# Optimization experiments

Measured on AMD Instinct MI355X. Metric: run time of the kernel, lower is better.

The kernel has to match this reference:

```python
import jax, jax.numpy as jnp
import numpy as np

N_NODES = 100000
N_EDGES = 1600000
N_FEAT = 64
DIM = 32
N_CLASSES = 10
N_GRAPHS = 64
BN_EPS = 1e-5


def setup_inputs() -> dict:
    key = jax.random.key(0)
    ks = jax.random.split(key, 20)
    x = jax.random.normal(ks[0], (N_NODES, N_FEAT), dtype=jnp.float32)
    edge_index = jax.random.randint(ks[1], (2, N_EDGES), 0, N_NODES, dtype=jnp.int64)
    batch = jnp.sort(jax.random.randint(ks[2], (N_NODES,), 0, N_GRAPHS, dtype=jnp.int64))
    s = 0.1
    # conv1 MLP (in=N_FEAT)
    w1a = jax.random.normal(ks[3], (N_FEAT, DIM), dtype=jnp.float32) * s
    b1a = jnp.zeros((DIM,), jnp.float32)
    w1b = jax.random.normal(ks[4], (DIM, DIM), dtype=jnp.float32) * s
    b1b = jnp.zeros((DIM,), jnp.float32)
    # convs 2-5 MLPs stacked [4, DIM, DIM]
    Wa = jax.random.normal(ks[5], (4, DIM, DIM), dtype=jnp.float32) * s
    Ba = jnp.zeros((4, DIM), jnp.float32)
    Wb = jax.random.normal(ks[6], (4, DIM, DIM), dtype=jnp.float32) * s
    Bb = jnp.zeros((4, DIM), jnp.float32)
    bn_gamma = jnp.ones((5, DIM), jnp.float32)
    bn_beta = jnp.zeros((5, DIM), jnp.float32)
    fc1_w = jax.random.normal(ks[7], (DIM, DIM), dtype=jnp.float32) * s
    fc1_b = jnp.zeros((DIM,), jnp.float32)
    fc2_w = jax.random.normal(ks[8], (DIM, N_CLASSES), dtype=jnp.float32) * s
    fc2_b = jnp.zeros((N_CLASSES,), jnp.float32)
    return dict(x=x, edge_index=edge_index, batch=batch,
                w1a=w1a, b1a=b1a, w1b=w1b, b1b=b1b,
                Wa=Wa, Ba=Ba, Wb=Wb, Bb=Bb,
                bn_gamma=bn_gamma, bn_beta=bn_beta,
                fc1_w=fc1_w, fc1_b=fc1_b, fc2_w=fc2_w, fc2_b=fc2_b)


def _gin_aggr(x, src, dst):
    # sum_{j in N(i)} x_j  + x_i   (eps = 0)
    agg = jax.ops.segment_sum(x[src], dst, num_segments=N_NODES)
    return x + agg


def _mlp(h, wa, ba, wb, bb):
    return jax.nn.relu(h @ wa + ba) @ wb + bb


def _bn(h, gamma, beta):
    mu = jnp.mean(h, axis=0)
    var = jnp.mean((h - mu) ** 2, axis=0)  # biased, torch BN training mode
    return (h - mu) * jax.lax.rsqrt(var + BN_EPS) * gamma + beta


def reference(x, edge_index, batch, w1a, b1a, w1b, b1b, Wa, Ba, Wb, Bb,
              bn_gamma, bn_beta, fc1_w, fc1_b, fc2_w, fc2_b):
    src, dst = edge_index[0], edge_index[1]
    # layer 1 (num_features -> dim)
    h = _mlp(_gin_aggr(x, src, dst), w1a, b1a, w1b, b1b)
    h = _bn(jax.nn.relu(h), bn_gamma[0], bn_beta[0])
    # layers 2-5 (dim -> dim)
    for i in range(4):
        h = _mlp(_gin_aggr(h, src, dst), Wa[i], Ba[i], Wb[i], Bb[i])
        h = _bn(jax.nn.relu(h), bn_gamma[i + 1], bn_beta[i + 1])
    # global add pool over graphs
    g = jax.ops.segment_sum(h, batch, num_segments=N_GRAPHS)  # [G, dim]
    g = jax.nn.relu(g @ fc1_w + fc1_b)
    # dropout: eval mode -> identity
    return g @ fc2_w + fc2_b  # [G, num_classes]
```

## Files before the change

kernel.cpp:

```cpp
#include <hip/hip_runtime.h>
#include <hip/hip_fp16.h>

#define NN 100000
#define NE 1600000
#define NF 64
#define DM 32
#define NG 64
#define NC 10
#define BN_EPS 1e-5f

#define BSHIFT 8
#define NBUCK ((NN + 255) >> 8)
#define CHUNK 8192
#define NCH ((NE + CHUNK - 1) / CHUNK)

__device__ __forceinline__ float2 up2(unsigned u) {
    __half2 h = __builtin_bit_cast(__half2, u);
    return __half22float2(h);
}
__device__ __forceinline__ unsigned pk2(float a, float b) {
    __half2 h = __floats2half2_rn(a, b);
    return __builtin_bit_cast(unsigned, h);
}

__global__ __launch_bounds__(256) void binA_k(const int* __restrict__ ei,
                                              int* __restrict__ bcnt) {
    __shared__ int h[NBUCK];
    for (int i = threadIdx.x; i < NBUCK; i += 256) h[i] = 0;
    __syncthreads();
    long long base = (long long)blockIdx.x * CHUNK;
    int n = (int)((NE - base < CHUNK) ? (NE - base) : CHUNK);
    for (int i = threadIdx.x; i < n; i += 256) {
        int d = ei[NE + base + i];
        atomicAdd(&h[d >> BSHIFT], 1);
    }
    __syncthreads();
    for (int i = threadIdx.x; i < NBUCK; i += 256)
        if (h[i]) atomicAdd(&bcnt[i], h[i]);
}

__global__ __launch_bounds__(512) void binB_k(const int* __restrict__ bcnt,
                                              int* __restrict__ bbase,
                                              int* __restrict__ bcur) {
    __shared__ int s[512];
    int t = threadIdx.x;
    int v = (t < NBUCK) ? bcnt[t] : 0;
    s[t] = v;
    __syncthreads();
    int acc = v;
    for (int off = 1; off < 512; off <<= 1) {
        int add = (t >= off) ? s[t - off] : 0;
        __syncthreads();
        acc += add;
        s[t] = acc;
        __syncthreads();
    }
    if (t < NBUCK) { bbase[t] = acc - v; bcur[t] = acc - v; }
    if (t == 0) bbase[NBUCK] = NE;
}

__global__ __launch_bounds__(256) void binC_k(const int* __restrict__ ei,
                                              int* __restrict__ bcur,
                                              unsigned* __restrict__ binned) {
    __shared__ int cnt[NBUCK];
    __shared__ int ofs[NBUCK];
    __shared__ int idx[NBUCK];
    for (int i = threadIdx.x; i < NBUCK; i += 256) { cnt[i] = 0; idx[i] = 0; }
    __syncthreads();
    long long base = (long long)blockIdx.x * CHUNK;
    int n = (int)((NE - base < CHUNK) ? (NE - base) : CHUNK);
    int d[CHUNK / 256];
#pragma unroll
    for (int k = 0; k < CHUNK / 256; k++) {
        int i = threadIdx.x + k * 256;
        int dd = (i < n) ? ei[NE + base + i] : -1;
        d[k] = dd;
        if (dd >= 0) atomicAdd(&cnt[dd >> BSHIFT], 1);
    }
    __syncthreads();
    for (int i = threadIdx.x; i < NBUCK; i += 256)
        if (cnt[i]) ofs[i] = atomicAdd(&bcur[i], cnt[i]);
    __syncthreads();
#pragma unroll
    for (int k = 0; k < CHUNK / 256; k++) {
        int i = threadIdx.x + k * 256;
        if (i < n) {
            unsigned src = (unsigned)ei[base + i];
            int b = d[k] >> BSHIFT;
            int l = atomicAdd(&idx[b], 1);
            binned[ofs[b] + l] = (src << 8) | (unsigned)(d[k] & 255);
        }
    }
}

__global__ __launch_bounds__(256) void binD_k(const unsigned* __restrict__ binned,
                                              const int* __restrict__ bbase,
                                              int* __restrict__ rowptr,
                                              int* __restrict__ csr) {
    __shared__ int cnt[256];
    __shared__ int cur[256];
    __shared__ int s[256];
    int b = blockIdx.x;
    int e0 = bbase[b], e1 = bbase[b + 1];
    int t = threadIdx.x;
    cnt[t] = 0;
    __syncthreads();
    for (int e = e0 + t; e < e1; e += 256) atomicAdd(&cnt[binned[e] & 255u], 1);
    __syncthreads();
    int v = cnt[t];
    s[t] = v;
    __syncthreads();
    int acc = v;
    for (int off = 1; off < 256; off <<= 1) {
        int add = (t >= off) ? s[t - off] : 0;
        __syncthreads();
        acc += add;
        s[t] = acc;
        __syncthreads();
    }
    int base = e0 + acc - v;
    int node = (b << BSHIFT) + t;
    if (node < NN) rowptr[node] = base;
    cur[t] = base;
    if (b == NBUCK - 1 && t == 0) rowptr[NN] = NE;
    __syncthreads();
    for (int e = e0 + t; e < e1; e += 256) {
        unsigned w = binned[e];
        int p = atomicAdd(&cur[w & 255u], 1);
        csr[p] = (int)(w >> 8);
    }
}

__global__ __launch_bounds__(256) void pre1_k(const float* __restrict__ x,
                                              const float* __restrict__ wa,
                                              float* __restrict__ y,
                                              unsigned* __restrict__ yhf,
                                              float* __restrict__ zbuf) {
    __shared__ float sWa[64 * 32];
    int tid = threadIdx.x;
    if (blockIdx.x == 0) {
        for (int i = tid; i < 5 * 64 + NG * 32; i += 256) zbuf[i] = 0.f;
    }
    for (int i = tid; i < 64 * 32; i += 256) sWa[i] = wa[i];
    __syncthreads();
    int l = tid & 3;
    int node = blockIdx.x * 64 + (tid >> 2);
    if (node >= NN) return;
    float t[8];
#pragma unroll
    for (int j = 0; j < 8; j++) t[j] = 0.f;
    const float4* xr = reinterpret_cast<const float4*>(x + (long long)node * 64);
    const float4* w4 = reinterpret_cast<const float4*>(sWa);
#pragma unroll
    for (int k4 = 0; k4 < 16; k4++) {
        float4 xv = xr[k4];
        float av[4] = {xv.x, xv.y, xv.z, xv.w};
#pragma unroll
        for (int i = 0; i < 4; i++) {
            float a = av[i];
            float4 w0 = w4[(k4 * 4 + i) * 8 + 2 * l];
            float4 w1 = w4[(k4 * 4 + i) * 8 + 2 * l + 1];
            t[0] += a * w0.x; t[1] += a * w0.y; t[2] += a * w0.z; t[3] += a * w0.w;
            t[4] += a * w1.x; t[5] += a * w1.y; t[6] += a * w1.z; t[7] += a * w1.w;
        }
    }
    float4* yr = reinterpret_cast<float4*>(y + (long long)node * 32 + l * 8);
    float4 o0, o1;
    o0.x = t[0]; o0.y = t[1]; o0.z = t[2]; o0.w = t[3];
    o1.x = t[4]; o1.y = t[5]; o1.z = t[6]; o1.w = t[7];
    yr[0] = o0; yr[1] = o1;
    uint4 p;
    p.x = pk2(t[0], t[1]); p.y = pk2(t[2], t[3]);
    p.z = pk2(t[4], t[5]); p.w = pk2(t[6], t[7]);
    reinterpret_cast<uint4*>(yhf)[(long long)node * 4 + l] = p;
}

template <bool BN>
__global__ __launch_bounds__(256) void gatherH_k(const unsigned* __restrict__ thf,
                                                 const int* __restrict__ rowptr,
                                                 const int* __restrict__ csr,
                                                 float* __restrict__ agg,
                                                 const float* __restrict__ st,
                                                 const float* __restrict__ gamma,
                                                 const float* __restrict__ beta) {
    int tid = threadIdx.x;
    int node = blockIdx.x * 64 + (tid >> 2);
    int l = tid & 3;
    if (node >= NN) return;
    float sc[8], sh[8];
    if (BN) {
        const float invn = 1.0f / NN;
#pragma unroll
        for (int c = 0; c < 8; c++) {
            int f = 8 * l + c;
            float mu = st[f] * invn;
            float var = st[32 + f] * invn - mu * mu;
            float scale = rsqrtf(var + BN_EPS) * gamma[f];
            sc[c] = scale;
            sh[c] = beta[f] - mu * scale;
        }
    }
    int s = rowptr[node], e = rowptr[node + 1];
    const uint4* t4 = reinterpret_cast<const uint4*>(thf);
    float a[8];
#pragma unroll
    for (int c = 0; c < 8; c++) a[c] = 0.f;
    int i = s;
    for (; i + 4 <= e; i += 4) {
        int s0 = csr[i], s1 = csr[i + 1], s2 = csr[i + 2], s3 = csr[i + 3];
        uint4 w0 = t4[(long long)s0 * 4 + l];
        uint4 w1 = t4[(long long)s1 * 4 + l];
        uint4 w2 = t4[(long long)s2 * 4 + l];
        uint4 w3 = t4[(long long)s3 * 4 + l];
        float2 p;
        p = up2(w0.x); a[0] += p.x; a[1] += p.y;
        p = up2(w0.y); a[2] += p.x; a[3] += p.y;
        p = up2(w0.z); a[4] += p.x; a[5] += p.y;
        p = up2(w0.w); a[6] += p.x; a[7] += p.y;
        p = up2(w1.x); a[0] += p.x; a[1] += p.y;
        p = up2(w1.y); a[2] += p.x; a[3] += p.y;
        p = up2(w1.z); a[4] += p.x; a[5] += p.y;
        p = up2(w1.w); a[6] += p.x; a[7] += p.y;
        p = up2(w2.x); a[0] += p.x; a[1] += p.y;
        p = up2(w2.y); a[2] += p.x; a[3] += p.y;
        p = up2(w2.z); a[4] += p.x; a[5] += p.y;
        p = up2(w2.w); a[6] += p.x; a[7] += p.y;
        p = up2(w3.x); a[0] += p.x; a[1] += p.y;
        p = up2(w3.y); a[2] += p.x; a[3] += p.y;
        p = up2(w3.z); a[4] += p.x; a[5] += p.y;
        p = up2(w3.w); a[6] += p.x; a[7] += p.y;
    }
    for (; i < e; i++) {
        uint4 w = t4[(long long)csr[i] * 4 + l];
        float2 p;
        p = up2(w.x); a[0] += p.x; a[1] += p.y;
        p = up2(w.y); a[2] += p.x; a[3] += p.y;
        p = up2(w.z); a[4] += p.x; a[5] += p.y;
        p = up2(w.w); a[6] += p.x; a[7] += p.y;
    }
    if (BN) {
        float deg = (float)(e - s);
#pragma unroll
        for (int c = 0; c < 8; c++) a[c] = a[c] * sc[c] + deg * sh[c];
    }
    float4* ar = reinterpret_cast<float4*>(agg + (long long)node * 32 + l * 8);
    float4 o0, o1;
    o0.x = a[0]; o0.y = a[1]; o0.z = a[2]; o0.w = a[3];
    o1.x = a[4]; o1.y = a[5]; o1.z = a[6]; o1.w = a[7];
    ar[0] = o0;
    ar[1] = o1;
}

__global__ __launch_bounds__(256) void mlp1b_k(const float* __restrict__ y,
                                               const float* __restrict__ agg,
                                               const float* __restrict__ ba,
                                               const float* __restrict__ wb,
                                               const float* __restrict__ bb,
                                               float* __restrict__ out,
                                               unsigned* __restrict__ outhf,
                                               float* __restrict__ stats) {
    __shared__ float sWb[32 * 32];
    __shared__ float sBa[32], sBb[32];
    __shared__ float sSum[4 * 32], sSq[4 * 32];
    int tid = threadIdx.x;
    for (int i = tid; i < 32 * 32; i += 256) sWb[i] = wb[i];
    if (tid < 32) { sBa[tid] = ba[tid]; sBb[tid] = bb[tid]; }
    __syncthreads();

    int l = tid & 3;
    int node = blockIdx.x * 64 + (tid >> 2);
    bool act = node < NN;
    float t[8];
    if (act) {
        const float4* yr = reinterpret_cast<const float4*>(y + (long long)node * 32 + l * 8);
        const float4* ar = reinterpret_cast<const float4*>(agg + (long long)node * 32 + l * 8);
        float4 y0 = yr[0], y1 = yr[1], a0 = ar[0], a1 = ar[1];
        t[0] = fmaxf(y0.x + a0.x + sBa[l * 8 + 0], 0.f);
        t[1] = fmaxf(y0.y + a0.y + sBa[l * 8 + 1], 0.f);
        t[2] = fmaxf(y0.z + a0.z + sBa[l * 8 + 2], 0.f);
        t[3] = fmaxf(y0.w + a0.w + sBa[l * 8 + 3], 0.f);
        t[4] = fmaxf(y1.x + a1.x + sBa[l * 8 + 4], 0.f);
        t[5] = fmaxf(y1.y + a1.y + sBa[l * 8 + 5], 0.f);
        t[6] = fmaxf(y1.z + a1.z + sBa[l * 8 + 6], 0.f);
        t[7] = fmaxf(y1.w + a1.w + sBa[l * 8 + 7], 0.f);
    } else {
#pragma unroll
        for (int j = 0; j < 8; j++) t[j] = 0.f;
    }

    float r[8];
#pragma unroll
    for (int j = 0; j < 8; j++) r[j] = sBb[l * 8 + j];
    const float4* v4 = reinterpret_cast<const float4*>(sWb);
#pragma unroll
    for (int k = 0; k < 32; k++) {
        float a = __shfl(t[k & 7], k >> 3, 4);
        float4 w0 = v4[k * 8 + 2 * l];
        float4 w1 = v4[k * 8 + 2 * l + 1];
        r[0] += a * w0.x; r[1] += a * w0.y; r[2] += a * w0.z; r[3] += a * w0.w;
        r[4] += a * w1.x; r[5] += a * w1.y; r[6] += a * w1.z; r[7] += a * w1.w;
    }
#pragma unroll
    for (int j = 0; j < 8; j++) r[j] = fmaxf(r[j], 0.f);

    if (act) {
        float4* orow = reinterpret_cast<float4*>(out + (long long)node * 32 + l * 8);
        float4 o0, o1;
        o0.x = r[0]; o0.y = r[1]; o0.z = r[2]; o0.w = r[3];
        o1.x = r[4]; o1.y = r[5]; o1.z = r[6]; o1.w = r[7];
        orow[0] = o0; orow[1] = o1;
        uint4 p;
        p.x = pk2(r[0], r[1]); p.y = pk2(r[2], r[3]);
        p.z = pk2(r[4], r[5]); p.w = pk2(r[6], r[7]);
        reinterpret_cast<uint4*>(outhf)[(long long)node * 4 + l] = p;
    } else {
#pragma unroll
        for (int j = 0; j < 8; j++) r[j] = 0.f;
    }

    int lane = tid & 63, wid = tid >> 6;
#pragma unroll
    for (int j = 0; j < 8; j++) {
        float v = r[j], v2 = v * v;
        v += __shfl_down(v, 32, 64); v2 += __shfl_down(v2, 32, 64);
        v += __shfl_down(v, 16, 64); v2 += __shfl_down(v2, 16, 64);
        v += __shfl_down(v, 8, 64);  v2 += __shfl_down(v2, 8, 64);
        v += __shfl_down(v, 4, 64);  v2 += __shfl_down(v2, 4, 64);
        if (lane < 4) { sSum[wid * 32 + lane * 8 + j] = v; sSq[wid * 32 + lane * 8 + j] = v2; }
    }
    __syncthreads();
    if (tid < 32) {
        float a = sSum[tid] + sSum[32 + tid] + sSum[64 + tid] + sSum[96 + tid];
        float b = sSq[tid] + sSq[32 + tid] + sSq[64 + tid] + sSq[96 + tid];
        atomicAdd(&stats[tid], a);
        atomicAdd(&stats[32 + tid], b);
    }
}

__global__ __launch_bounds__(256) void mlp32_bn_k(float* __restrict__ h,
                                                  unsigned* __restrict__ hhf,
                                                  const float* __restrict__ agg,
                                                  const float* __restrict__ wa,
                                                  const float* __restrict__ ba,
                                                  const float* __restrict__ wb,
                                                  const float* __restrict__ bb,
                                                  const float* __restrict__ st,
                                                  const float* __restrict__ gamma,
                                                  const float* __restrict__ beta,
                                                  float* __restrict__ statsOut) {
    __shared__ float sWa[32 * 32];
    __shared__ float sWb[32 * 32];
    __shared__ float sBa[32], sBb[32];
    __shared__ float sSc[32], sSh[32];
    __shared__ float sSum[4 * 32], sSq[4 * 32];
    int tid = threadIdx.x;
    for (int i = tid; i < 32 * 32; i += 256) { sWa[i] = wa[i]; sWb[i] = wb[i]; }
    if (tid < 32) {
        sBa[tid] = ba[tid]; sBb[tid] = bb[tid];
        const float invn = 1.0f / NN;
        float mu = st[tid] * invn;
        float var = st[32 + tid] * invn - mu * mu;
        float scale = rsqrtf(var + BN_EPS) * gamma[tid];
        sSc[tid] = scale;
        sSh[tid] = beta[tid] - mu * scale;
    }
    __syncthreads();

    int l = tid & 3;
    int node = blockIdx.x * 64 + (tid >> 2);
    bool act = node < NN;
    float t[8];
    const float4* w4a = reinterpret_cast<const float4*>(sWa);
    if (act) {
        float a[32];
        const float4* hr = reinterpret_cast<const float4*>(h + (long long)node * 32);
        const float4* ar = reinterpret_cast<const float4*>(agg + (long long)node * 32);
#pragma unroll
        for (int k4 = 0; k4 < 8; k4++) {
            float4 xv = hr[k4];
            float4 av = ar[k4];
            a[k4 * 4 + 0] = xv.x * sSc[k4 * 4 + 0] + sSh[k4 * 4 + 0] + av.x;
            a[k4 * 4 + 1] = xv.y * sSc[k4 * 4 + 1] + sSh[k4 * 4 + 1] + av.y;
            a[k4 * 4 + 2] = xv.z * sSc[k4 * 4 + 2] + sSh[k4 * 4 + 2] + av.z;
            a[k4 * 4 + 3] = xv.w * sSc[k4 * 4 + 3] + sSh[k4 * 4 + 3] + av.w;
        }
#pragma unroll
        for (int j = 0; j < 8; j++) t[j] = sBa[l * 8 + j];
#pragma unroll
        for (int k = 0; k < 32; k++) {
            float av = a[k];
            float4 w0 = w4a[k * 8 + 2 * l];
            float4 w1 = w4a[k * 8 + 2 * l + 1];
            t[0] += av * w0.x; t[1] += av * w0.y; t[2] += av * w0.z; t[3] += av * w0.w;
            t[4] += av * w1.x; t[5] += av * w1.y; t[6] += av * w1.z; t[7] += av * w1.w;
        }
#pragma unroll
        for (int j = 0; j < 8; j++) t[j] = fmaxf(t[j], 0.f);
    } else {
#pragma unroll
        for (int j = 0; j < 8; j++) t[j] = 0.f;
    }

    float r[8];
#pragma unroll
    for (int j = 0; j < 8; j++) r[j] = sBb[l * 8 + j];
    const float4* v4 = reinterpret_cast<const float4*>(sWb);
#pragma unroll
    for (int k = 0; k < 32; k++) {
        float a = __shfl(t[k & 7], k >> 3, 4);
        float4 w0 = v4[k * 8 + 2 * l];
        float4 w1 = v4[k * 8 + 2 * l + 1];
        r[0] += a * w0.x; r[1] += a * w0.y; r[2] += a * w0.z; r[3] += a * w0.w;
        r[4] += a * w1.x; r[5] += a * w1.y; r[6] += a * w1.z; r[7] += a * w1.w;
    }
#pragma unroll
    for (int j = 0; j < 8; j++) r[j] = fmaxf(r[j], 0.f);

    if (act) {
        float4* orow = reinterpret_cast<float4*>(h + (long long)node * 32 + l * 8);
        float4 o0, o1;
        o0.x = r[0]; o0.y = r[1]; o0.z = r[2]; o0.w = r[3];
        o1.x = r[4]; o1.y = r[5]; o1.z = r[6]; o1.w = r[7];
        orow[0] = o0; orow[1] = o1;
        uint4 p;
        p.x = pk2(r[0], r[1]); p.y = pk2(r[2], r[3]);
        p.z = pk2(r[4], r[5]); p.w = pk2(r[6], r[7]);
        reinterpret_cast<uint4*>(hhf)[(long long)node * 4 + l] = p;
    } else {
#pragma unroll
        for (int j = 0; j < 8; j++) r[j] = 0.f;
    }

    int lane = tid & 63, wid = tid >> 6;
#pragma unroll
    for (int j = 0; j < 8; j++) {
        float v = r[j], v2 = v * v;
        v += __shfl_down(v, 32, 64); v2 += __shfl_down(v2, 32, 64);
        v += __shfl_down(v, 16, 64); v2 += __shfl_down(v2, 16, 64);
        v += __shfl_down(v, 8, 64);  v2 += __shfl_down(v2, 8, 64);
        v += __shfl_down(v, 4, 64);  v2 += __shfl_down(v2, 4, 64);
        if (lane < 4) { sSum[wid * 32 + lane * 8 + j] = v; sSq[wid * 32 + lane * 8 + j] = v2; }
    }
    __syncthreads();
    if (tid < 32) {
        float a = sSum[tid] + sSum[32 + tid] + sSum[64 + tid] + sSum[96 + tid];
        float b = sSq[tid] + sSq[32 + tid] + sSq[64 + tid] + sSq[96 + tid];
        atomicAdd(&statsOut[tid], a);
        atomicAdd(&statsOut[32 + tid], b);
    }
}

#define POOL_NPB 512
__global__ __launch_bounds__(256) void pool_bn_k(const float* __restrict__ h,
                                                 const int* __restrict__ batch,
                                                 const float* __restrict__ st,
                                                 const float* __restrict__ gamma,
                                                 const float* __restrict__ beta,
                                                 float* __restrict__ pooled) {
    int tid = threadIdx.x;
    int f = tid & 31;
    int p = tid >> 5;
    int n0 = blockIdx.x * POOL_NPB + p * (POOL_NPB / 8);
    int n1 = n0 + POOL_NPB / 8;
    if (n1 > NN) n1 = NN;
    if (n0 >= NN) return;
    const float invn = 1.0f / NN;
    float mu = st[f] * invn;
    float var = st[32 + f] * invn - mu * mu;
    float sc = rsqrtf(var + BN_EPS) * gamma[f];
    float sh = beta[f] - mu * sc;
    float acc = 0.f;
    int cur = batch[n0];
    for (int n = n0; n < n1; n++) {
        int g = batch[n];
        if (g != cur) {
            atomicAdd(&pooled[cur * 32 + f], acc);
            cur = g;
            acc = 0.f;
        }
        acc += h[(long long)n * 32 + f] * sc + sh;
    }
    atomicAdd(&pooled[cur * 32 + f], acc);
}

__global__ __launch_bounds__(64) void final_k(const float* __restrict__ pooled,
                                              const float* __restrict__ w1,
                                              const float* __restrict__ b1,
                                              const float* __restrict__ w2,
                                              const float* __restrict__ b2,
                                              float* __restrict__ out) {
    int g = threadIdx.x;
    if (g >= NG) return;
    float t[32];
#pragma unroll
    for (int j = 0; j < 32; j++) t[j] = b1[j];
    for (int k = 0; k < 32; k++) {
        float a = pooled[g * 32 + k];
#pragma unroll
        for (int j = 0; j < 32; j++) t[j] += a * w1[k * 32 + j];
    }
#pragma unroll
    for (int j = 0; j < 32; j++) t[j] = fmaxf(t[j], 0.f);
    for (int c = 0; c < NC; c++) {
        float o = b2[c];
#pragma unroll
        for (int k = 0; k < 32; k++) o += t[k] * w2[k * NC + c];
        out[g * NC + c] = o;
    }
}

extern "C" void kernel_launch(void* const* d_in, const int* in_sizes, int n_in,
                              void* d_out, int out_size, void* d_ws, size_t ws_size,
                              hipStream_t stream) {
    const float* x = (const float*)d_in[0];
    const int* ei = (const int*)d_in[1];
    const int* batch = (const int*)d_in[2];
    const float* w1a = (const float*)d_in[3];
    const float* b1a = (const float*)d_in[4];
    const float* w1b = (const float*)d_in[5];
    const float* b1b = (const float*)d_in[6];
    const float* Wa = (const float*)d_in[7];
    const float* Ba = (const float*)d_in[8];
    const float* Wb = (const float*)d_in[9];
    const float* Bb = (const float*)d_in[10];
    const float* bn_gamma = (const float*)d_in[11];
    const float* bn_beta = (const float*)d_in[12];
    const float* fc1w = (const float*)d_in[13];
    const float* fc1b = (const float*)d_in[14];
    const float* fc2w = (const float*)d_in[15];
    const float* fc2b = (const float*)d_in[16];
    float* out = (float*)d_out;

    float* ws = (float*)d_ws;
    float* y = ws;
    float* hb = y + (size_t)NN * 32;
    float* agg = hb + (size_t)NN * 32;
    float* stats_all = agg + (size_t)NN * 32;
    float* pooled = stats_all + 5 * 64;
    unsigned* yhf = (unsigned*)(pooled + NG * 32);
    unsigned* hbhf = yhf + (size_t)NN * 16;
    unsigned* binned = hbhf + (size_t)NN * 16;
    int* bcnt = (int*)(binned + NE);
    int* bbase = bcnt + NBUCK;
    int* bcur = bbase + NBUCK + 1;
    int* rowptr = bcur + NBUCK;
    int* csr = rowptr + NN + 1;

    const int nb4 = (NN + 63) / 64;

    hipMemsetAsync(bcnt, 0, NBUCK * sizeof(int), stream);
    binA_k<<<NCH, 256, 0, stream>>>(ei, bcnt);
    binB_k<<<1, 512, 0, stream>>>(bcnt, bbase, bcur);
    binC_k<<<NCH, 256, 0, stream>>>(ei, bcur, binned);
    binD_k<<<NBUCK, 256, 0, stream>>>(binned, bbase, rowptr, csr);

    pre1_k<<<nb4, 256, 0, stream>>>(x, w1a, y, yhf, stats_all);
    gatherH_k<false><<<nb4, 256, 0, stream>>>(yhf, rowptr, csr, agg,
                                              nullptr, nullptr, nullptr);
    mlp1b_k<<<nb4, 256, 0, stream>>>(y, agg, b1a, w1b, b1b, hb, hbhf, stats_all);

    for (int i = 0; i < 4; i++) {
        const float* st = stats_all + i * 64;
        const float* g = bn_gamma + i * 32;
        const float* be = bn_beta + i * 32;
        gatherH_k<true><<<nb4, 256, 0, stream>>>(hbhf, rowptr, csr, agg, st, g, be);
        mlp32_bn_k<<<nb4, 256, 0, stream>>>(hb, hbhf, agg, Wa + i * 1024, Ba + i * 32,
                                            Wb + i * 1024, Bb + i * 32,
                                            st, g, be, stats_all + (i + 1) * 64);
    }

    pool_bn_k<<<(NN + POOL_NPB - 1) / POOL_NPB, 256, 0, stream>>>(
        hb, batch, stats_all + 4 * 64, bn_gamma + 4 * 32, bn_beta + 4 * 32, pooled);
    final_k<<<1, 64, 0, stream>>>(pooled, fc1w, fc1b, fc2w, fc2b, out);
}
```

Measured before the change: 584.0 us.

## Fuse neighbor gather with per-layer MLP and BN into one kernel

Merges the CSR gather kernel with the following MLP/BN kernel for every layer, so the aggregated features stay in registers and shared memory instead of being written to and re-read from a global agg buffer. The fp16 gather tables are ping-ponged between two buffers because each layer now reads one table while writing the next. The node's 32-wide input row is staged through a padded shared-memory transpose for the matvecs. This saves one fp32 round trip of the activations and one launch per layer. In exchange each block holds more shared memory and registers, and adds extra barriers between the gather and the MLP phases.

```diff
diff --git a/kernel.cpp b/kernel.cpp
--- a/kernel.cpp
+++ b/kernel.cpp
@@ -175,36 +175,57 @@
     reinterpret_cast<uint4*>(yhf)[(long long)node * 4 + l] = p;
 }
 
-template <bool BN>
-__global__ __launch_bounds__(256) void gatherH_k(const unsigned* __restrict__ thf,
-                                                 const int* __restrict__ rowptr,
-                                                 const int* __restrict__ csr,
-                                                 float* __restrict__ agg,
-                                                 const float* __restrict__ st,
-                                                 const float* __restrict__ gamma,
-                                                 const float* __restrict__ beta) {
+#define SSTR 65
+template <int MODE>
+__global__ __launch_bounds__(256) void fused_k(const float* __restrict__ selfRow,
+                                               float* __restrict__ hOut,
+                                               const unsigned* __restrict__ tblIn,
+                                               unsigned* __restrict__ tblOut,
+                                               const int* __restrict__ rowptr,
+                                               const int* __restrict__ csr,
+                                               const float* __restrict__ wa,
+                                               const float* __restrict__ ba,
+                                               const float* __restrict__ wb,
+                                               const float* __restrict__ bb,
+                                               const float* __restrict__ stPrev,
+                                               const float* __restrict__ gammaPrev,
+                                               const float* __restrict__ betaPrev,
+                                               float* __restrict__ statsOut) {
+    __shared__ float sWa[32 * 32];
+    __shared__ float sWb[32 * 32];
+    __shared__ float sBa[32], sBb[32];
+    __shared__ float sSc[32], sSh[32];
+    __shared__ float sStage[32 * SSTR];
+    __shared__ float sSum[4 * 32], sSq[4 * 32];
     int tid = threadIdx.x;
-    int node = blockIdx.x * 64 + (tid >> 2);
+    for (int i = tid; i < 32 * 32; i += 256) {
+        sWb[i] = wb[i];
+        if (MODE) sWa[i] = wa[i];
+    }
+    if (tid < 32) {
+        sBa[tid] = ba[tid];
+        sBb[tid] = bb[tid];
+        if (MODE) {
+            const float invn = 1.0f / NN;
+            float mu = stPrev[tid] * invn;
+            float var = stPrev[32 + tid] * invn - mu * mu;
+            float scale = rsqrtf(var + BN_EPS) * gammaPrev[tid];
+            sSc[tid] = scale;
+            sSh[tid] = betaPrev[tid] - mu * scale;
+        }
+    }
+
     int l = tid & 3;
-    if (node >= NN) return;
-    float sc[8], sh[8];
-    if (BN) {
-        const float invn = 1.0f / NN;
-#pragma unroll
-        for (int c = 0; c < 8; c++) {
-            int f = 8 * l + c;
-            float mu = st[f] * invn;
-            float var = st[32 + f] * invn - mu * mu;
-            float scale = rsqrtf(var + BN_EPS) * gamma[f];
-            sc[c] = scale;
-            sh[c] = beta[f] - mu * scale;
-        }
-    }
-    int s = rowptr[node], e = rowptr[node + 1];
-    const uint4* t4 = reinterpret_cast<const uint4*>(thf);
-    float a[8];
-#pragma unroll
-    for (int c = 0; c < 8; c++) a[c] = 0.f;
+    int nl = tid >> 2;
+    int node = blockIdx.x * 64 + nl;
+    bool act = node < NN;
+
+    int s = 0, e = 0;
+    if (act) { s = rowptr[node]; e = rowptr[node + 1]; }
+    const uint4* t4 = reinterpret_cast<const uint4*>(tblIn);
+    float g[8];
+#pragma unroll
+    for (int c = 0; c < 8; c++) g[c] = 0.f;
     int i = s;
     for (; i + 4 <= e; i += 4) {
         int s0 = csr[i], s1 = csr[i + 1], s2 = csr[i + 2], s3 = csr[i + 3];
@@ -213,90 +234,92 @@
         uint4 w2 = t4[(long long)s2 * 4 + l];
         uint4 w3 = t4[(long long)s3 * 4 + l];
         float2 p;
-        p = up2(w0.x); a[0] += p.x; a[1] += p.y;
-        p = up2(w0.y); a[2] += p.x; a[3] += p.y;
-        p = up2(w0.z); a[4] += p.x; a[5] += p.y;
-        p = up2(w0.w); a[6] += p.x; a[7] += p.y;
-        p = up2(w1.x); a[0] += p.x; a[1] += p.y;
-        p = up2(w1.y); a[2] += p.x; a[3] += p.y;
-        p = up2(w1.z); a[4] += p.x; a[5] += p.y;
-        p = up2(w1.w); a[6] += p.x; a[7] += p.y;
-        p = up2(w2.x); a[0] += p.x; a[1] += p.y;
-        p = up2(w2.y); a[2] += p.x; a[3] += p.y;
-        p = up2(w2.z); a[4] += p.x; a[5] += p.y;
-        p = up2(w2.w); a[6] += p.x; a[7] += p.y;
-        p = up2(w3.x); a[0] += p.x; a[1] += p.y;
-        p = up2(w3.y); a[2] += p.x; a[3] += p.y;
-        p = up2(w3.z); a[4] += p.x; a[5] += p.y;
-        p = up2(w3.w); a[6] += p.x; a[7] += p.y;
+        p = up2(w0.x); g[0] += p.x; g[1] += p.y;
+        p = up2(w0.y); g[2] += p.x; g[3] += p.y;
+        p = up2(w0.z); g[4] += p.x; g[5] += p.y;
+        p = up2(w0.w); g[6] += p.x; g[7] += p.y;
+        p = up2(w1.x); g[0] += p.x; g[1] += p.y;
+        p = up2(w1.y); g[2] += p.x; g[3] += p.y;
+        p = up2(w1.z); g[4] += p.x; g[5] += p.y;
+        p = up2(w1.w); g[6] += p.x; g[7] += p.y;
+        p = up2(w2.x); g[0] += p.x; g[1] += p.y;
+        p = up2(w2.y); g[2] += p.x; g[3] += p.y;
+        p = up2(w2.z); g[4] += p.x; g[5] += p.y;
+        p = up2(w2.w); g[6] += p.x; g[7] += p.y;
+        p = up2(w3.x); g[0] += p.x; g[1] += p.y;
+        p = up2(w3.y); g[2] += p.x; g[3] += p.y;
+        p = up2(w3.z); g[4] += p.x; g[5] += p.y;
+        p = up2(w3.w); g[6] += p.x; g[7] += p.y;
     }
     for (; i < e; i++) {
         uint4 w = t4[(long long)csr[i] * 4 + l];
         float2 p;
-        p = up2(w.x); a[0] += p.x; a[1] += p.y;
-        p = up2(w.y); a[2] += p.x; a[3] += p.y;
-        p = up2(w.z); a[4] += p.x; a[5] += p.y;
-        p = up2(w.w); a[6] += p.x; a[7] += p.y;
-    }
-    if (BN) {
-        float deg = (float)(e - s);
-#pragma unroll
-        for (int c = 0; c < 8; c++) a[c] = a[c] * sc[c] + deg * sh[c];
-    }
-    float4* ar = reinterpret_cast<float4*>(agg + (long long)node * 32 + l * 8);
-    float4 o0, o1;
-    o0.x = a[0]; o0.y = a[1]; o0.z = a[2]; o0.w = a[3];
-    o1.x = a[4]; o1.y = a[5]; o1.z = a[6]; o1.w = a[7];
-    ar[0] = o0;
-    ar[1] = o1;
-}
-
-__global__ __launch_bounds__(256) void mlp1b_k(const float* __restrict__ y,
-                                               const float* __restrict__ agg,
-                                               const float* __restrict__ ba,
-                                               const float* __restrict__ wb,
-                                               const float* __restrict__ bb,
-                                               float* __restrict__ out,
-                                               unsigned* __restrict__ outhf,
-                                               float* __restrict__ stats) {
-    __shared__ float sWb[32 * 32];
-    __shared__ float sBa[32], sBb[32];
-    __shared__ float sSum[4 * 32], sSq[4 * 32];
-    int tid = threadIdx.x;
-    for (int i = tid; i < 32 * 32; i += 256) sWb[i] = wb[i];
-    if (tid < 32) { sBa[tid] = ba[tid]; sBb[tid] = bb[tid]; }
-    __syncthreads();
-
-    int l = tid & 3;
-    int node = blockIdx.x * 64 + (tid >> 2);
-    bool act = node < NN;
+        p = up2(w.x); g[0] += p.x; g[1] += p.y;
+        p = up2(w.y); g[2] += p.x; g[3] += p.y;
+        p = up2(w.z); g[4] += p.x; g[5] += p.y;
+        p = up2(w.w); g[6] += p.x; g[7] += p.y;
+    }
+    __syncthreads();
+
     float t[8];
-    if (act) {
-        const float4* yr = reinterpret_cast<const float4*>(y + (long long)node * 32 + l * 8);
-        const float4* ar = reinterpret_cast<const float4*>(agg + (long long)node * 32 + l * 8);
-        float4 y0 = yr[0], y1 = yr[1], a0 = ar[0], a1 = ar[1];
-        t[0] = fmaxf(y0.x + a0.x + sBa[l * 8 + 0], 0.f);
-        t[1] = fmaxf(y0.y + a0.y + sBa[l * 8 + 1], 0.f);
-        t[2] = fmaxf(y0.z + a0.z + sBa[l * 8 + 2], 0.f);
-        t[3] = fmaxf(y0.w + a0.w + sBa[l * 8 + 3], 0.f);
-        t[4] = fmaxf(y1.x + a1.x + sBa[l * 8 + 4], 0.f);
-        t[5] = fmaxf(y1.y + a1.y + sBa[l * 8 + 5], 0.f);
-        t[6] = fmaxf(y1.z + a1.z + sBa[l * 8 + 6], 0.f);
-        t[7] = fmaxf(y1.w + a1.w + sBa[l * 8 + 7], 0.f);
+    if (MODE) {
+        float in[8];
+        if (act) {
+            const float4* hr = reinterpret_cast<const float4*>(selfRow + (long long)node * 32 + l * 8);
+            float4 h0 = hr[0], h1 = hr[1];
+            float deg = (float)(e - s);
+            float hv[8] = {h0.x, h0.y, h0.z, h0.w, h1.x, h1.y, h1.z, h1.w};
+#pragma unroll
+            for (int c = 0; c < 8; c++) {
+                int f = l * 8 + c;
+                in[c] = hv[c] * sSc[f] + sSh[f] + (g[c] * sSc[f] + deg * sSh[f]);
+            }
+        } else {
+#pragma unroll
+            for (int c = 0; c < 8; c++) in[c] = 0.f;
+        }
+#pragma unroll
+        for (int c = 0; c < 8; c++) sStage[(l * 8 + c) * SSTR + nl] = in[c];
+        __syncthreads();
+#pragma unroll
+        for (int j = 0; j < 8; j++) t[j] = sBa[l * 8 + j];
+        const float4* w4a = reinterpret_cast<const float4*>(sWa);
+#pragma unroll
+        for (int k = 0; k < 32; k++) {
+            float a = sStage[k * SSTR + nl];
+            float4 w0 = w4a[k * 8 + 2 * l];
+            float4 w1 = w4a[k * 8 + 2 * l + 1];
+            t[0] += a * w0.x; t[1] += a * w0.y; t[2] += a * w0.z; t[3] += a * w0.w;
+            t[4] += a * w1.x; t[5] += a * w1.y; t[6] += a * w1.z; t[7] += a * w1.w;
+        }
+#pragma unroll
+        for (int j = 0; j < 8; j++) t[j] = fmaxf(t[j], 0.f);
+        __syncthreads();
     } else {
-#pragma unroll
-        for (int j = 0; j < 8; j++) t[j] = 0.f;
-    }
-
+        if (act) {
+            const float4* yr = reinterpret_cast<const float4*>(selfRow + (long long)node * 32 + l * 8);
+            float4 y0 = yr[0], y1 = yr[1];
+            float yv[8] = {y0.x, y0.y, y0.z, y0.w, y1.x, y1.y, y1.z, y1.w};
+#pragma unroll
+            for (int c = 0; c < 8; c++) t[c] = fmaxf(yv[c] + g[c] + sBa[l * 8 + c], 0.f);
+        } else {
+#pragma unroll
+            for (int c = 0; c < 8; c++) t[c] = 0.f;
+        }
+    }
+
+#pragma unroll
+    for (int c = 0; c < 8; c++) sStage[(l * 8 + c) * SSTR + nl] = t[c];
+    __syncthreads();
     float r[8];
 #pragma unroll
     for (int j = 0; j < 8; j++) r[j] = sBb[l * 8 + j];
-    const float4* v4 = reinterpret_cast<const float4*>(sWb);
+    const float4* w4b = reinterpret_cast<const float4*>(sWb);
 #pragma unroll
     for (int k = 0; k < 32; k++) {
-        float a = __shfl(t[k & 7], k >> 3, 4);
-        float4 w0 = v4[k * 8 + 2 * l];
-        float4 w1 = v4[k * 8 + 2 * l + 1];
+        float a = sStage[k * SSTR + nl];
+        float4 w0 = w4b[k * 8 + 2 * l];
+        float4 w1 = w4b[k * 8 + 2 * l + 1];
         r[0] += a * w0.x; r[1] += a * w0.y; r[2] += a * w0.z; r[3] += a * w0.w;
         r[4] += a * w1.x; r[5] += a * w1.y; r[6] += a * w1.z; r[7] += a * w1.w;
     }
@@ -304,7 +327,7 @@
     for (int j = 0; j < 8; j++) r[j] = fmaxf(r[j], 0.f);
 
     if (act) {
-        float4* orow = reinterpret_cast<float4*>(out + (long long)node * 32 + l * 8);
+        float4* orow = reinterpret_cast<float4*>(hOut + (long long)node * 32 + l * 8);
         float4 o0, o1;
         o0.x = r[0]; o0.y = r[1]; o0.z = r[2]; o0.w = r[3];
         o1.x = r[4]; o1.y = r[5]; o1.z = r[6]; o1.w = r[7];
@@ -312,120 +335,7 @@
         uint4 p;
         p.x = pk2(r[0], r[1]); p.y = pk2(r[2], r[3]);
         p.z = pk2(r[4], r[5]); p.w = pk2(r[6], r[7]);
-        reinterpret_cast<uint4*>(outhf)[(long long)node * 4 + l] = p;
-    } else {
-#pragma unroll
-        for (int j = 0; j < 8; j++) r[j] = 0.f;
-    }
-
-    int lane = tid & 63, wid = tid >> 6;
-#pragma unroll
-    for (int j = 0; j < 8; j++) {
-        float v = r[j], v2 = v * v;
-        v += __shfl_down(v, 32, 64); v2 += __shfl_down(v2, 32, 64);
-        v += __shfl_down(v, 16, 64); v2 += __shfl_down(v2, 16, 64);
-        v += __shfl_down(v, 8, 64);  v2 += __shfl_down(v2, 8, 64);
-        v += __shfl_down(v, 4, 64);  v2 += __shfl_down(v2, 4, 64);
-        if (lane < 4) { sSum[wid * 32 + lane * 8 + j] = v; sSq[wid * 32 + lane * 8 + j] = v2; }
-    }
-    __syncthreads();
-    if (tid < 32) {
-        float a = sSum[tid] + sSum[32 + tid] + sSum[64 + tid] + sSum[96 + tid];
-        float b = sSq[tid] + sSq[32 + tid] + sSq[64 + tid] + sSq[96 + tid];
-        atomicAdd(&stats[tid], a);
-        atomicAdd(&stats[32 + tid], b);
-    }
-}
-
-__global__ __launch_bounds__(256) void mlp32_bn_k(float* __restrict__ h,
-                                                  unsigned* __restrict__ hhf,
-                                                  const float* __restrict__ agg,
-                                                  const float* __restrict__ wa,
-                                                  const float* __restrict__ ba,
-                                                  const float* __restrict__ wb,
-                                                  const float* __restrict__ bb,
-                                                  const float* __restrict__ st,
-                                                  const float* __restrict__ gamma,
-                                                  const float* __restrict__ beta,
-                                                  float* __restrict__ statsOut) {
-    __shared__ float sWa[32 * 32];
-    __shared__ float sWb[32 * 32];
-    __shared__ float sBa[32], sBb[32];
-    __shared__ float sSc[32], sSh[32];
-    __shared__ float sSum[4 * 32], sSq[4 * 32];
-    int tid = threadIdx.x;
-    for (int i = tid; i < 32 * 32; i += 256) { sWa[i] = wa[i]; sWb[i] = wb[i]; }
-    if (tid < 32) {
-        sBa[tid] = ba[tid]; sBb[tid] = bb[tid];
-        const float invn = 1.0f / NN;
-        float mu = st[tid] * invn;
-        float var = st[32 + tid] * invn - mu * mu;
-        float scale = rsqrtf(var + BN_EPS) * gamma[tid];
-        sSc[tid] = scale;
-        sSh[tid] = beta[tid] - mu * scale;
-    }
-    __syncthreads();
-
-    int l = tid & 3;
-    int node = blockIdx.x * 64 + (tid >> 2);
-    bool act = node < NN;
-    float t[8];
-    const float4* w4a = reinterpret_cast<const float4*>(sWa);
-    if (act) {
-        float a[32];
-        const float4* hr = reinterpret_cast<const float4*>(h + (long long)node * 32);
-        const float4* ar = reinterpret_cast<const float4*>(agg + (long long)node * 32);
-#pragma unroll
-        for (int k4 = 0; k4 < 8; k4++) {
-            float4 xv = hr[k4];
-            float4 av = ar[k4];
-            a[k4 * 4 + 0] = xv.x * sSc[k4 * 4 + 0] + sSh[k4 * 4 + 0] + av.x;
-            a[k4 * 4 + 1] = xv.y * sSc[k4 * 4 + 1] + sSh[k4 * 4 + 1] + av.y;
-            a[k4 * 4 + 2] = xv.z * sSc[k4 * 4 + 2] + sSh[k4 * 4 + 2] + av.z;
-            a[k4 * 4 + 3] = xv.w * sSc[k4 * 4 + 3] + sSh[k4 * 4 + 3] + av.w;
-        }
-#pragma unroll
-        for (int j = 0; j < 8; j++) t[j] = sBa[l * 8 + j];
-#pragma unroll
-        for (int k = 0; k < 32; k++) {
-            float av = a[k];
-            float4 w0 = w4a[k * 8 + 2 * l];
-            float4 w1 = w4a[k * 8 + 2 * l + 1];
-            t[0] += av * w0.x; t[1] += av * w0.y; t[2] += av * w0.z; t[3] += av * w0.w;
-            t[4] += av * w1.x; t[5] += av * w1.y; t[6] += av * w1.z; t[7] += av * w1.w;
-        }
-#pragma unroll
-        for (int j = 0; j < 8; j++) t[j] = fmaxf(t[j], 0.f);
-    } else {
-#pragma unroll
-        for (int j = 0; j < 8; j++) t[j] = 0.f;
-    }
-
-    float r[8];
-#pragma unroll
-    for (int j = 0; j < 8; j++) r[j] = sBb[l * 8 + j];
-    const float4* v4 = reinterpret_cast<const float4*>(sWb);
-#pragma unroll
-    for (int k = 0; k < 32; k++) {
-        float a = __shfl(t[k & 7], k >> 3, 4);
-        float4 w0 = v4[k * 8 + 2 * l];
-        float4 w1 = v4[k * 8 + 2 * l + 1];
-        r[0] += a * w0.x; r[1] += a * w0.y; r[2] += a * w0.z; r[3] += a * w0.w;
-        r[4] += a * w1.x; r[5] += a * w1.y; r[6] += a * w1.z; r[7] += a * w1.w;
-    }
-#pragma unroll
-    for (int j = 0; j < 8; j++) r[j] = fmaxf(r[j], 0.f);
-
-    if (act) {
-        float4* orow = reinterpret_cast<float4*>(h + (long long)node * 32 + l * 8);
-        float4 o0, o1;
-        o0.x = r[0]; o0.y = r[1]; o0.z = r[2]; o0.w = r[3];
-        o1.x = r[4]; o1.y = r[5]; o1.z = r[6]; o1.w = r[7];
-        orow[0] = o0; orow[1] = o1;
-        uint4 p;
-        p.x = pk2(r[0], r[1]); p.y = pk2(r[2], r[3]);
-        p.z = pk2(r[4], r[5]); p.w = pk2(r[6], r[7]);
-        reinterpret_cast<uint4*>(hhf)[(long long)node * 4 + l] = p;
+        reinterpret_cast<uint4*>(tblOut)[(long long)node * 4 + l] = p;
     } else {
 #pragma unroll
         for (int j = 0; j < 8; j++) r[j] = 0.f;
@@ -534,12 +444,12 @@
     float* ws = (float*)d_ws;
     float* y = ws;
     float* hb = y + (size_t)NN * 32;
-    float* agg = hb + (size_t)NN * 32;
-    float* stats_all = agg + (size_t)NN * 32;
+    float* stats_all = hb + (size_t)NN * 32;
     float* pooled = stats_all + 5 * 64;
     unsigned* yhf = (unsigned*)(pooled + NG * 32);
-    unsigned* hbhf = yhf + (size_t)NN * 16;
-    unsigned* binned = hbhf + (size_t)NN * 16;
+    unsigned* hfA = yhf + (size_t)NN * 16;
+    unsigned* hfB = hfA + (size_t)NN * 16;
+    unsigned* binned = hfB + (size_t)NN * 16;
     int* bcnt = (int*)(binned + NE);
     int* bbase = bcnt + NBUCK;
     int* bcur = bbase + NBUCK + 1;
@@ -555,18 +465,19 @@
     binD_k<<<NBUCK, 256, 0, stream>>>(binned, bbase, rowptr, csr);
 
     pre1_k<<<nb4, 256, 0, stream>>>(x, w1a, y, yhf, stats_all);
-    gatherH_k<false><<<nb4, 256, 0, stream>>>(yhf, rowptr, csr, agg,
-                                              nullptr, nullptr, nullptr);
-    mlp1b_k<<<nb4, 256, 0, stream>>>(y, agg, b1a, w1b, b1b, hb, hbhf, stats_all);
-
+    fused_k<0><<<nb4, 256, 0, stream>>>(y, hb, yhf, hfA, rowptr, csr,
+                                        nullptr, b1a, w1b, b1b,
+                                        nullptr, nullptr, nullptr, stats_all);
+
+    unsigned* tin = hfA;
+    unsigned* tout = hfB;
     for (int i = 0; i < 4; i++) {
-        const float* st = stats_all + i * 64;
-        const float* g = bn_gamma + i * 32;
-        const float* be = bn_beta + i * 32;
-        gatherH_k<true><<<nb4, 256, 0, stream>>>(hbhf, rowptr, csr, agg, st, g, be);
-        mlp32_bn_k<<<nb4, 256, 0, stream>>>(hb, hbhf, agg, Wa + i * 1024, Ba + i * 32,
+        fused_k<1><<<nb4, 256, 0, stream>>>(hb, hb, tin, tout, rowptr, csr,
+                                            Wa + i * 1024, Ba + i * 32,
                                             Wb + i * 1024, Bb + i * 32,
-                                            st, g, be, stats_all + (i + 1) * 64);
+                                            stats_all + i * 64, bn_gamma + i * 32,
+                                            bn_beta + i * 32, stats_all + (i + 1) * 64);
+        unsigned* tmp = tin; tin = tout; tout = tmp;
     }
 
     pool_bn_k<<<(NN + POOL_NPB - 1) / POOL_NPB, 256, 0, stream>>>(
```

New measurement: 528.3 us. 1.11x faster.
